# Kernel tuning notes

Measured on AMD Instinct MI355X. Metric: run time of the kernel, lower is better.

Reference implementation:

```python
import jax, jax.numpy as jnp
import numpy as np

N = 384          # nodes per graph
HID = 128        # hid_dim
H = 8            # shared_num_heads
C = HID // H     # shared_head_dim = 16
L = 4            # num_layers
VOCAB = 20
NORB = 4
NCAT = NORB * NORB + NORB   # 20 edge categories
OUT = 10
B = 4
E = N * N        # fully-connected closure incl. self loops
EPS = 1e-5


def layer_norm(x, g, b):
    m = jnp.mean(x, axis=-1, keepdims=True)
    v = jnp.mean((x - m) ** 2, axis=-1, keepdims=True)
    return (x - m) / jnp.sqrt(v + EPS) * g + b


def setup_inputs() -> dict:
    key = jax.random.key(0)
    ks = iter(jax.random.split(key, 32))

    def nrm(shape, s=0.05):
        return jax.random.normal(next(ks), shape, jnp.float32) * s

    # edge structure: fully connected, edge (i,j) in row-major order
    pos = np.arange(N) % NORB                    # node -> orbit
    src = np.repeat(np.arange(N), N)
    tgt = np.tile(np.arange(N), N)
    cat = np.where(src == tgt, NORB * NORB + pos[src], pos[src] * NORB + pos[tgt])

    x = jax.random.randint(next(ks), (B, N, 1), 0, VOCAB, jnp.int32)

    return dict(
        x=x,
        edge_src=jnp.asarray(src, jnp.int32),
        edge_tgt=jnp.asarray(tgt, jnp.int32),
        edge_cat=jnp.asarray(cat, jnp.int32),
        token_emb=nrm((VOCAB, HID), 1.0),
        edge_emb=nrm((NCAT, HID), 1.0),
        ln_in1_g=jnp.ones((HID,), jnp.float32), ln_in1_b=jnp.zeros((HID,), jnp.float32),
        W_in=nrm((HID, HID)), b_in=jnp.zeros((HID,), jnp.float32),
        ln_in2_g=jnp.ones((HID,), jnp.float32), ln_in2_b=jnp.zeros((HID,), jnp.float32),
        Wl=nrm((L, HID, H * C)), bl=jnp.zeros((L, H * C), jnp.float32),
        Wr=nrm((L, HID, H * C)), br=jnp.zeros((L, H * C), jnp.float32),
        We=nrm((L, HID, H * C)),                           # lin_edge has no bias in PyG GATv2Conv
        att=nrm((L, H, C)),
        bias_gat=jnp.zeros((L, H * C), jnp.float32),
        W_proj=nrm((L, HID, HID)), b_proj=jnp.zeros((L, HID), jnp.float32),
        ln_g=jnp.ones((L, HID), jnp.float32), ln_b=jnp.zeros((L, HID), jnp.float32),
        W_out=nrm((HID, OUT)), b_out=jnp.zeros((OUT,), jnp.float32),
    )


def reference(x, edge_src, edge_tgt, edge_cat,
              token_emb, edge_emb,
              ln_in1_g, ln_in1_b, W_in, b_in, ln_in2_g, ln_in2_b,
              Wl, bl, Wr, br, We, att, bias_gat,
              W_proj, b_proj, ln_g, ln_b, W_out, b_out):
    edge_feat = edge_emb[edge_cat]                       # [E, HID] gather by category
    h = token_emb[x[..., 0]]                             # [B, N, HID]
    # input MLP: LN -> ReLU -> Linear -> LN
    h = layer_norm(h, ln_in1_g, ln_in1_b)
    h = jax.nn.relu(h)
    h = h @ W_in + b_in
    h = layer_norm(h, ln_in2_g, ln_in2_b)

    for l in range(L):
        edge_e = (edge_feat @ We[l]).reshape(E, H, C)    # shared across batch

        def conv(hb):  # hb: [N, HID]  GATv2Conv, concat heads
            xl = (hb @ Wl[l] + bl[l]).reshape(N, H, C)   # source transform
            xr = (hb @ Wr[l] + br[l]).reshape(N, H, C)   # target transform
            e = jax.nn.leaky_relu(xl[edge_src] + xr[edge_tgt] + edge_e, 0.2)  # [E,H,C]
            logits = jnp.einsum('ehc,hc->eh', e, att[l])                      # [E,H]
            # segment softmax over edges sharing a target node
            m = jax.ops.segment_max(logits, edge_tgt, num_segments=N)
            ex = jnp.exp(logits - m[edge_tgt])
            den = jax.ops.segment_sum(ex, edge_tgt, num_segments=N)
            alpha = ex / den[edge_tgt]                                        # [E,H]
            out = jax.ops.segment_sum(xl[edge_src] * alpha[:, :, None], edge_tgt,
                                      num_segments=N)                         # [N,H,C]
            return out.reshape(N, H * C) + bias_gat[l]

        h_prev = h
        h = jax.vmap(conv)(h)                            # [B, N, HID]
        h = h @ W_proj[l] + b_proj[l]
        h = layer_norm(h, ln_g[l], ln_b[l])
        h = jax.nn.relu(h) + h_prev                      # residual

    h = h.sum(axis=1)                                    # sum over nodes -> [B, HID]
    return h @ W_out + b_out                             # [B, OUT]
```

## Files before the change

kernel.cpp:

```cpp
#include <hip/hip_runtime.h>


#define NN 384
#define NB 4
#define TJ 4

__device__ __forceinline__ void reduce64(float& a, float& b) {
#pragma unroll
  for (int m = 1; m <= 32; m <<= 1) {
    a += __shfl_xor(a, m, 64);
    b += __shfl_xor(b, m, 64);
  }
}

__global__ __launch_bounds__(256) void k_init(
    const int* __restrict__ x,
    const float* __restrict__ token_emb, const float* __restrict__ edge_emb,
    const float* __restrict__ ln1g, const float* __restrict__ ln1b,
    const float* __restrict__ W_in, const float* __restrict__ b_in,
    const float* __restrict__ ln2g, const float* __restrict__ ln2b,
    const float* __restrict__ Wl, const float* __restrict__ bl,
    const float* __restrict__ Wr, const float* __restrict__ br,
    const float* __restrict__ We, const float* __restrict__ att_w,
    float* __restrict__ ce, float* __restrict__ h,
    float* __restrict__ xl, float* __restrict__ xr, float* __restrict__ datt0)
{
  const int blk = blockIdx.x, t = threadIdx.x;
  if (blk < 40) {
    const int idx = blk * 256 + t;
    const int hc = idx & 127, rest = idx >> 7;
    const int cat = rest % 20, l = rest / 20;
    const float* er = edge_emb + cat * 128;
    const float* w  = We + (l * 128) * 128 + hc;
    float acc = 0.f;
#pragma unroll 8
    for (int k = 0; k < 128; ++k) acc = fmaf(er[k], w[k * 128], acc);
    ce[idx] = acc;
    return;
  }
  __shared__ float trow[4][128];
  __shared__ float hbuf[4][128];
  const int r0 = (blk - 40) * 4;
  const int r = t >> 6, c2 = (t & 63) * 2;
  const int row = r0 + r;
  const int tok = x[row];
  float2 v = *(const float2*)(token_emb + tok * 128 + c2);
  float s1 = v.x + v.y;
  float s2 = v.x * v.x + v.y * v.y;
  reduce64(s1, s2);
  float mean = s1 * 0.0078125f;
  float inv  = rsqrtf(s2 * 0.0078125f - mean * mean + 1e-5f);
  {
    float2 g  = *(const float2*)(ln1g + c2);
    float2 bb = *(const float2*)(ln1b + c2);
    trow[r][c2 + 0] = fmaxf((v.x - mean) * inv * g.x + bb.x, 0.f);
    trow[r][c2 + 1] = fmaxf((v.y - mean) * inv * g.y + bb.y, 0.f);
  }
  __syncthreads();
  const int o = t & 127, rh = (t >> 7) * 2;
  {
    float a0, a1;
    { float bo = b_in[o]; a0 = a1 = bo; }
    for (int k = 0; k < 128; ++k) {
      float w = W_in[k * 128 + o];
      a0 = fmaf(trow[rh + 0][k], w, a0);
      a1 = fmaf(trow[rh + 1][k], w, a1);
    }
    hbuf[rh + 0][o] = a0; hbuf[rh + 1][o] = a1;
  }
  __syncthreads();
  v = *(const float2*)(&hbuf[r][c2]);
  s1 = v.x + v.y;
  s2 = v.x * v.x + v.y * v.y;
  reduce64(s1, s2);
  mean = s1 * 0.0078125f;
  inv  = rsqrtf(s2 * 0.0078125f - mean * mean + 1e-5f);
  {
    float2 g  = *(const float2*)(ln2g + c2);
    float2 bb = *(const float2*)(ln2b + c2);
    float2 hv;
    hv.x = (v.x - mean) * inv * g.x + bb.x;
    hv.y = (v.y - mean) * inv * g.y + bb.y;
    trow[r][c2] = hv.x; trow[r][c2 + 1] = hv.y;
    *(float2*)(h + row * 128 + c2) = hv;
  }
  __syncthreads();
  const int m = t >> 7;
  const float* W = m ? Wr : Wl;
  const float bias = (m ? br : bl)[o];
  float a0 = bias, a1 = bias, a2 = bias, a3 = bias;
  for (int k = 0; k < 128; ++k) {
    float wv = W[k * 128 + o];
    a0 = fmaf(trow[0][k], wv, a0);
    a1 = fmaf(trow[1][k], wv, a1);
    a2 = fmaf(trow[2][k], wv, a2);
    a3 = fmaf(trow[3][k], wv, a3);
  }
  float* dst = m ? xr : xl;
  dst[(r0 + 0) * 128 + o] = a0;
  dst[(r0 + 1) * 128 + o] = a1;
  dst[(r0 + 2) * 128 + o] = a2;
  dst[(r0 + 3) * 128 + o] = a3;
  if (m == 0) {
    float av = att_w[o];
    float s0 = av * a0, sA = av * a1, sB = av * a2, sC = av * a3;
#pragma unroll
    for (int mm = 1; mm <= 8; mm <<= 1) {
      s0 += __shfl_xor(s0, mm, 64);
      sA += __shfl_xor(sA, mm, 64);
      sB += __shfl_xor(sB, mm, 64);
      sC += __shfl_xor(sC, mm, 64);
    }
    if ((t & 15) == 0) {
      const int hh2 = o >> 4;
      const int b2 = r0 / NN, ii = r0 - b2 * NN;
      const int base = (b2 * 8 + hh2) * NN + ii;
      datt0[base + 0] = s0; datt0[base + 1] = sA;
      datt0[base + 2] = sB; datt0[base + 3] = sC;
    }
  }
}

__global__ __launch_bounds__(256) void k_layer(
    const float* __restrict__ xl_in, const float* __restrict__ xr_in,
    const float* __restrict__ datt_in,
    float* __restrict__ xl_out, float* __restrict__ xr_out,
    float* __restrict__ datt_out,
    float* __restrict__ h, const float* __restrict__ ce,
    const float* __restrict__ att_w, const float* __restrict__ bias_gat,
    const float* __restrict__ W_proj, const float* __restrict__ b_proj,
    const float* __restrict__ ln_g, const float* __restrict__ ln_b,
    const float* __restrict__ Wl, const float* __restrict__ bl,
    const float* __restrict__ Wr, const float* __restrict__ br,
    int l, int next_l)
{
  __shared__ float xrce[TJ][5][136];
  __shared__ float djr02[TJ][5][8];
  __shared__ float mbuf[8][32][17];
  __shared__ float arow[TJ][132];
  __shared__ float pbuf[2 * TJ][132];
  __shared__ float nrow[TJ][132];

  const int t = threadIdx.x;
  const int jt = blockIdx.x, b = blockIdx.y;
  const int j0 = jt * TJ;

  for (int idx = t; idx < TJ * 5 * 128; idx += 256) {
    const int hc = idx & 127, rest = idx >> 7;
    const int sel = rest % 5, jj = rest / 5;
    const int j = j0 + jj, pj = j & 3;
    const int cat = (sel == 4) ? (16 + pj) : (sel * 4 + pj);
    xrce[jj][sel][hc] = xr_in[(b * NN + j) * 128 + hc]
                      + ce[(l * 20 + cat) * 128 + hc];
  }
  __syncthreads();
  if (t < TJ * 5 * 8) {
    const int jj = t / 40, r2 = t % 40, sel = r2 >> 3, h2 = r2 & 7;
    float d = 0.f;
#pragma unroll
    for (int c = 0; c < 16; ++c)
      d += xrce[jj][sel][h2 * 16 + c] * att_w[l * 128 + h2 * 16 + c];
    djr02[jj][sel][h2] = 0.2f * d;
  }
  __syncthreads();

  const int hh = t >> 5, isub = t & 31;
  float attv[16];
  {
    const float* ap = att_w + l * 128 + hh * 16;
#pragma unroll
    for (int c = 0; c < 16; ++c) attv[c] = ap[c];
  }
  float sden[TJ];
  float acc[TJ][16];
#pragma unroll
  for (int jj = 0; jj < TJ; ++jj) {
    sden[jj] = 0.f;
#pragma unroll
    for (int c = 0; c < 16; ++c) acc[jj][c] = 0.f;
  }
  const float* xlb = xl_in + (b * NN) * 128 + hh * 16;
  const float* dp  = datt_in + (b * 8 + hh) * NN;

#pragma unroll 2
  for (int it = 0; it < NN / 32; ++it) {
    const int i = isub + 32 * it;
    float xv[16];
    {
      const float4* xp = (const float4*)(xlb + i * 128);
#pragma unroll
      for (int q = 0; q < 4; ++q) {
        float4 a = xp[q];
        xv[q * 4 + 0] = a.x; xv[q * 4 + 1] = a.y;
        xv[q * 4 + 2] = a.z; xv[q * 4 + 3] = a.w;
      }
    }
    const float di02 = 0.2f * dp[i];
    const int pi = i & 3;
#pragma unroll
    for (int jj = 0; jj < TJ; ++jj) {
      const int sel = (i == j0 + jj) ? 4 : pi;
      const float4* bp = (const float4*)(&xrce[jj][sel][hh * 16]);
      float p = 0.f;
#pragma unroll
      for (int q = 0; q < 4; ++q) {
        float4 cv = bp[q];
        p = fmaf(fmaxf(xv[q * 4 + 0] + cv.x, 0.f), attv[q * 4 + 0], p);
        p = fmaf(fmaxf(xv[q * 4 + 1] + cv.y, 0.f), attv[q * 4 + 1], p);
        p = fmaf(fmaxf(xv[q * 4 + 2] + cv.z, 0.f), attv[q * 4 + 2], p);
        p = fmaf(fmaxf(xv[q * 4 + 3] + cv.w, 0.f), attv[q * 4 + 3], p);
      }
      const float e = __expf(fmaf(0.8f, p, di02 + djr02[jj][sel][hh]));
      sden[jj] += e;
#pragma unroll
      for (int c = 0; c < 16; ++c) acc[jj][c] = fmaf(e, xv[c], acc[jj][c]);
    }
  }

  {
    const int lc = isub & 15, up = isub >> 4;
#pragma unroll
    for (int jj = 0; jj < TJ; ++jj) {
      mbuf[hh][isub][0] = sden[jj];
#pragma unroll
      for (int c = 0; c < 16; ++c) mbuf[hh][isub][1 + c] = acc[jj][c];
      float nsum = 0.f, dsum = 0.f;
#pragma unroll 4
      for (int u2 = 0; u2 < 16; ++u2) {
        const int u = up * 16 + u2;
        dsum += mbuf[hh][u][0];
        nsum += mbuf[hh][u][1 + lc];
      }
      nsum += __shfl_xor(nsum, 16, 64); dsum += __shfl_xor(dsum, 16, 64);
      if (isub < 16)
        arow[jj][hh * 16 + isub] =
            nsum / dsum + bias_gat[l * 128 + hh * 16 + isub];
    }
  }
  __syncthreads();

  {
    const int o = t & 127, g4 = t >> 7;
    const float* Wp = W_proj + l * 16384;
    float p0 = 0.f, p1 = 0.f, p2 = 0.f, p3 = 0.f;
    const int k0 = g4 * 64;
    for (int kk = 0; kk < 64; ++kk) {
      const int k = k0 + kk;
      const float w = Wp[k * 128 + o];
      p0 = fmaf(arow[0][k], w, p0);
      p1 = fmaf(arow[1][k], w, p1);
      p2 = fmaf(arow[2][k], w, p2);
      p3 = fmaf(arow[3][k], w, p3);
    }
    pbuf[g4 * TJ + 0][o] = p0;
    pbuf[g4 * TJ + 1][o] = p1;
    pbuf[g4 * TJ + 2][o] = p2;
    pbuf[g4 * TJ + 3][o] = p3;
  }
  __syncthreads();
  for (int idx = t; idx < TJ * 128; idx += 256) {
    const int rr = idx >> 7, o = idx & 127;
    nrow[rr][o] = pbuf[rr][o] + pbuf[TJ + rr][o] + b_proj[l * 128 + o];
  }
  __syncthreads();

  {
    const int w = t >> 6;
    const int c2 = (t & 63) * 2;
    float v0 = nrow[w][c2], v1 = nrow[w][c2 + 1];
    float s1 = v0 + v1, s2 = v0 * v0 + v1 * v1;
#pragma unroll
    for (int m = 1; m <= 32; m <<= 1) {
      s1 += __shfl_xor(s1, m, 64);
      s2 += __shfl_xor(s2, m, 64);
    }
    const float mean = s1 * 0.0078125f;
    const float inv  = rsqrtf(s2 * 0.0078125f - mean * mean + 1e-5f);
    const int row = (b * NN + j0 + w) * 128;
    const float g0 = ln_g[l * 128 + c2], g1 = ln_g[l * 128 + c2 + 1];
    const float b0 = ln_b[l * 128 + c2], b1 = ln_b[l * 128 + c2 + 1];
    const float hp0 = h[row + c2], hp1 = h[row + c2 + 1];
    const float hn0 = fmaxf((v0 - mean) * inv * g0 + b0, 0.f) + hp0;
    const float hn1 = fmaxf((v1 - mean) * inv * g1 + b1, 0.f) + hp1;
    h[row + c2] = hn0; h[row + c2 + 1] = hn1;
    nrow[w][c2] = hn0; nrow[w][c2 + 1] = hn1;
  }
  __syncthreads();

  if (next_l >= 0) {
    const int o = t & 127, m = t >> 7;
    const float* W = (m ? Wr : Wl) + next_l * 16384;
    const float bias = (m ? br : bl)[next_l * 128 + o];
    float a0 = bias, a1 = bias, a2 = bias, a3 = bias;
    for (int k = 0; k < 128; ++k) {
      const float wv = W[k * 128 + o];
      a0 = fmaf(nrow[0][k], wv, a0);
      a1 = fmaf(nrow[1][k], wv, a1);
      a2 = fmaf(nrow[2][k], wv, a2);
      a3 = fmaf(nrow[3][k], wv, a3);
    }
    float* dst = m ? xr_out : xl_out;
    const int rb = (b * NN + j0) * 128 + o;
    dst[rb +   0] = a0; dst[rb + 128] = a1;
    dst[rb + 256] = a2; dst[rb + 384] = a3;
    if (m == 0) {
      const float av = att_w[next_l * 128 + o];
      float s0 = av * a0, s1 = av * a1, s2 = av * a2, s3 = av * a3;
#pragma unroll
      for (int mm = 1; mm <= 8; mm <<= 1) {
        s0 += __shfl_xor(s0, mm, 64);
        s1 += __shfl_xor(s1, mm, 64);
        s2 += __shfl_xor(s2, mm, 64);
        s3 += __shfl_xor(s3, mm, 64);
      }
      if ((t & 15) == 0) {
        const int base = (b * 8 + (o >> 4)) * NN + j0;
        datt_out[base + 0] = s0;
        datt_out[base + 1] = s1;
        datt_out[base + 2] = s2;
        datt_out[base + 3] = s3;
      }
    }
  }
}

__global__ __launch_bounds__(256) void k_final(
    const float* __restrict__ h, const float* __restrict__ W_out,
    const float* __restrict__ b_out, float* __restrict__ out)
{
  __shared__ float sbuf[2][128];
  const int bq = blockIdx.x, t = threadIdx.x;
  const int o = t & 127, half = t >> 7;
  float acc = 0.f;
  const float* hp = h + (bq * NN + half * 192) * 128 + o;
  for (int n = 0; n < 192; ++n) acc += hp[n * 128];
  sbuf[half][o] = acc;
  __syncthreads();
  if (t < 10) {
    float a = b_out[t];
#pragma unroll 8
    for (int k = 0; k < 128; ++k)
      a = fmaf(sbuf[0][k] + sbuf[1][k], W_out[k * 10 + t], a);
    out[bq * 10 + t] = a;
  }
}

extern "C" void kernel_launch(void* const* d_in, const int* in_sizes, int n_in,
                              void* d_out, int out_size, void* d_ws, size_t ws_size,
                              hipStream_t stream) {
  const int*   x         = (const int*)d_in[0];
  const float* token_emb = (const float*)d_in[4];
  const float* edge_emb  = (const float*)d_in[5];
  const float* ln1g      = (const float*)d_in[6];
  const float* ln1b      = (const float*)d_in[7];
  const float* W_in      = (const float*)d_in[8];
  const float* b_in      = (const float*)d_in[9];
  const float* ln2g      = (const float*)d_in[10];
  const float* ln2b      = (const float*)d_in[11];
  const float* Wl        = (const float*)d_in[12];
  const float* bl        = (const float*)d_in[13];
  const float* Wr        = (const float*)d_in[14];
  const float* br        = (const float*)d_in[15];
  const float* We        = (const float*)d_in[16];
  const float* att_w     = (const float*)d_in[17];
  const float* bias_gat  = (const float*)d_in[18];
  const float* W_proj    = (const float*)d_in[19];
  const float* b_proj    = (const float*)d_in[20];
  const float* ln_g      = (const float*)d_in[21];
  const float* ln_b      = (const float*)d_in[22];
  const float* W_out     = (const float*)d_in[23];
  const float* b_out     = (const float*)d_in[24];

  float* ws  = (float*)d_ws;
  float* ce  = ws;
  float* h   = ce  + 10240;
  float* xlA = h   + 196608;
  float* xrA = xlA + 196608;
  float* xlB = xrA + 196608;
  float* xrB = xlB + 196608;
  float* dA  = xrB + 196608;
  float* dB  = dA  + 12288;

  k_init<<<dim3(40 + 384), 256, 0, stream>>>(
      x, token_emb, edge_emb, ln1g, ln1b, W_in, b_in, ln2g, ln2b,
      Wl, bl, Wr, br, We, att_w, ce, h, xlA, xrA, dA);
  for (int l = 0; l < 4; ++l) {
    const bool even = (l & 1) == 0;
    float* xin  = even ? xlA : xlB;  float* rin  = even ? xrA : xrB;
    float* din  = even ? dA  : dB;
    float* xout = even ? xlB : xlA;  float* rout = even ? xrB : xrA;
    float* dout = even ? dB  : dA;
    k_layer<<<dim3(NN / TJ, NB), 256, 0, stream>>>(
        xin, rin, din, xout, rout, dout, h, ce, att_w, bias_gat,
        W_proj, b_proj, ln_g, ln_b, Wl, bl, Wr, br, l, (l < 3) ? l + 1 : -1);
  }
  k_final<<<dim3(NB), 256, 0, stream>>>(h, W_out, b_out, (float*)d_out);
}
```

Before: 236.9 us.

## Fuse init, layers and final into one persistent kernel with grid barriers

Merges the init kernel, the four per-layer kernels and the final reduction into a single persistent launch of 384 blocks. Stages are separated by a hand-written flag-based grid barrier built on agent-scope atomics. The goal is to remove the per-launch overhead and tail gaps of six kernel launches. The cost is barrier latency, and the design relies on all 384 blocks being co-resident (launch_bounds 256,2); without that the barrier could deadlock. It also needs flag reset at exit for the next call.

```diff
diff --git a/kernel.cpp b/kernel.cpp
--- a/kernel.cpp
+++ b/kernel.cpp
@@ -4,6 +4,36 @@
 #define NN 384
 #define NB 4
 #define TJ 4
+#define NJT 96
+#define NBLK 384
+
+__device__ unsigned g_flag[NBLK];
+__device__ unsigned g_rel;
+
+__device__ __forceinline__ void gridbar(int k, int blk, int t) {
+  __syncthreads();
+  __threadfence();
+  if (blk == 0) {
+    for (int s = 1 + t; s < NBLK; s += 256)
+      while (__hip_atomic_load(&g_flag[s], __ATOMIC_ACQUIRE,
+                               __HIP_MEMORY_SCOPE_AGENT) < (unsigned)k)
+        __builtin_amdgcn_s_sleep(2);
+    __syncthreads();
+    if (t == 0)
+      __hip_atomic_store(&g_rel, (unsigned)k, __ATOMIC_RELEASE,
+                         __HIP_MEMORY_SCOPE_AGENT);
+  } else {
+    if (t == 0) {
+      __hip_atomic_store(&g_flag[blk], (unsigned)k, __ATOMIC_RELEASE,
+                         __HIP_MEMORY_SCOPE_AGENT);
+      while (__hip_atomic_load(&g_rel, __ATOMIC_ACQUIRE,
+                               __HIP_MEMORY_SCOPE_AGENT) < (unsigned)k)
+        __builtin_amdgcn_s_sleep(2);
+    }
+  }
+  __syncthreads();
+  __threadfence();
+}
 
 __device__ __forceinline__ void reduce64(float& a, float& b) {
 #pragma unroll
@@ -13,7 +43,19 @@
   }
 }
 
-__global__ __launch_bounds__(256) void k_init(
+struct SmemLayer {
+  float xrce[TJ][5][136];
+  float djr02[TJ][5][8];
+  float mbuf[8][32][17];
+  float arow[TJ][132];
+  float pbuf[2 * TJ][132];
+  float nrow[TJ][132];
+};
+struct SmemInit  { float trow[4][128]; float hbuf[4][128]; };
+struct SmemFinal { float sbuf[2][128]; };
+union SmemU { SmemLayer L; SmemInit I; SmemFinal F; };
+
+__global__ __launch_bounds__(256, 2) void k_mega(
     const int* __restrict__ x,
     const float* __restrict__ token_emb, const float* __restrict__ edge_emb,
     const float* __restrict__ ln1g, const float* __restrict__ ln1b,
@@ -22,10 +64,24 @@
     const float* __restrict__ Wl, const float* __restrict__ bl,
     const float* __restrict__ Wr, const float* __restrict__ br,
     const float* __restrict__ We, const float* __restrict__ att_w,
-    float* __restrict__ ce, float* __restrict__ h,
-    float* __restrict__ xl, float* __restrict__ xr, float* __restrict__ datt0)
+    const float* __restrict__ bias_gat,
+    const float* __restrict__ W_proj, const float* __restrict__ b_proj,
+    const float* __restrict__ ln_g, const float* __restrict__ ln_b,
+    const float* __restrict__ W_out, const float* __restrict__ b_out,
+    float* __restrict__ ws, float* __restrict__ out)
 {
+  __shared__ SmemU smem;
+  float* ce  = ws;
+  float* h   = ce  + 10240;
+  float* xlA = h   + 196608;
+  float* xrA = xlA + 196608;
+  float* xlB = xrA + 196608;
+  float* xrB = xlB + 196608;
+  float* dA  = xrB + 196608;
+  float* dB  = dA  + 12288;
+
   const int blk = blockIdx.x, t = threadIdx.x;
+
   if (blk < 40) {
     const int idx = blk * 256 + t;
     const int hc = idx & 127, rest = idx >> 7;
@@ -36,312 +92,310 @@
 #pragma unroll 8
     for (int k = 0; k < 128; ++k) acc = fmaf(er[k], w[k * 128], acc);
     ce[idx] = acc;
-    return;
-  }
-  __shared__ float trow[4][128];
-  __shared__ float hbuf[4][128];
-  const int r0 = (blk - 40) * 4;
-  const int r = t >> 6, c2 = (t & 63) * 2;
-  const int row = r0 + r;
-  const int tok = x[row];
-  float2 v = *(const float2*)(token_emb + tok * 128 + c2);
-  float s1 = v.x + v.y;
-  float s2 = v.x * v.x + v.y * v.y;
-  reduce64(s1, s2);
-  float mean = s1 * 0.0078125f;
-  float inv  = rsqrtf(s2 * 0.0078125f - mean * mean + 1e-5f);
+  }
   {
-    float2 g  = *(const float2*)(ln1g + c2);
-    float2 bb = *(const float2*)(ln1b + c2);
-    trow[r][c2 + 0] = fmaxf((v.x - mean) * inv * g.x + bb.x, 0.f);
-    trow[r][c2 + 1] = fmaxf((v.y - mean) * inv * g.y + bb.y, 0.f);
-  }
-  __syncthreads();
-  const int o = t & 127, rh = (t >> 7) * 2;
-  {
-    float a0, a1;
-    { float bo = b_in[o]; a0 = a1 = bo; }
-    for (int k = 0; k < 128; ++k) {
-      float w = W_in[k * 128 + o];
-      a0 = fmaf(trow[rh + 0][k], w, a0);
-      a1 = fmaf(trow[rh + 1][k], w, a1);
-    }
-    hbuf[rh + 0][o] = a0; hbuf[rh + 1][o] = a1;
-  }
-  __syncthreads();
-  v = *(const float2*)(&hbuf[r][c2]);
-  s1 = v.x + v.y;
-  s2 = v.x * v.x + v.y * v.y;
-  reduce64(s1, s2);
-  mean = s1 * 0.0078125f;
-  inv  = rsqrtf(s2 * 0.0078125f - mean * mean + 1e-5f);
-  {
-    float2 g  = *(const float2*)(ln2g + c2);
-    float2 bb = *(const float2*)(ln2b + c2);
-    float2 hv;
-    hv.x = (v.x - mean) * inv * g.x + bb.x;
-    hv.y = (v.y - mean) * inv * g.y + bb.y;
-    trow[r][c2] = hv.x; trow[r][c2 + 1] = hv.y;
-    *(float2*)(h + row * 128 + c2) = hv;
-  }
-  __syncthreads();
-  const int m = t >> 7;
-  const float* W = m ? Wr : Wl;
-  const float bias = (m ? br : bl)[o];
-  float a0 = bias, a1 = bias, a2 = bias, a3 = bias;
-  for (int k = 0; k < 128; ++k) {
-    float wv = W[k * 128 + o];
-    a0 = fmaf(trow[0][k], wv, a0);
-    a1 = fmaf(trow[1][k], wv, a1);
-    a2 = fmaf(trow[2][k], wv, a2);
-    a3 = fmaf(trow[3][k], wv, a3);
-  }
-  float* dst = m ? xr : xl;
-  dst[(r0 + 0) * 128 + o] = a0;
-  dst[(r0 + 1) * 128 + o] = a1;
-  dst[(r0 + 2) * 128 + o] = a2;
-  dst[(r0 + 3) * 128 + o] = a3;
-  if (m == 0) {
-    float av = att_w[o];
-    float s0 = av * a0, sA = av * a1, sB = av * a2, sC = av * a3;
-#pragma unroll
-    for (int mm = 1; mm <= 8; mm <<= 1) {
-      s0 += __shfl_xor(s0, mm, 64);
-      sA += __shfl_xor(sA, mm, 64);
-      sB += __shfl_xor(sB, mm, 64);
-      sC += __shfl_xor(sC, mm, 64);
-    }
-    if ((t & 15) == 0) {
-      const int hh2 = o >> 4;
-      const int b2 = r0 / NN, ii = r0 - b2 * NN;
-      const int base = (b2 * 8 + hh2) * NN + ii;
-      datt0[base + 0] = s0; datt0[base + 1] = sA;
-      datt0[base + 2] = sB; datt0[base + 3] = sC;
-    }
-  }
-}
-
-__global__ __launch_bounds__(256) void k_layer(
-    const float* __restrict__ xl_in, const float* __restrict__ xr_in,
-    const float* __restrict__ datt_in,
-    float* __restrict__ xl_out, float* __restrict__ xr_out,
-    float* __restrict__ datt_out,
-    float* __restrict__ h, const float* __restrict__ ce,
-    const float* __restrict__ att_w, const float* __restrict__ bias_gat,
-    const float* __restrict__ W_proj, const float* __restrict__ b_proj,
-    const float* __restrict__ ln_g, const float* __restrict__ ln_b,
-    const float* __restrict__ Wl, const float* __restrict__ bl,
-    const float* __restrict__ Wr, const float* __restrict__ br,
-    int l, int next_l)
-{
-  __shared__ float xrce[TJ][5][136];
-  __shared__ float djr02[TJ][5][8];
-  __shared__ float mbuf[8][32][17];
-  __shared__ float arow[TJ][132];
-  __shared__ float pbuf[2 * TJ][132];
-  __shared__ float nrow[TJ][132];
-
-  const int t = threadIdx.x;
-  const int jt = blockIdx.x, b = blockIdx.y;
-  const int j0 = jt * TJ;
-
-  for (int idx = t; idx < TJ * 5 * 128; idx += 256) {
-    const int hc = idx & 127, rest = idx >> 7;
-    const int sel = rest % 5, jj = rest / 5;
-    const int j = j0 + jj, pj = j & 3;
-    const int cat = (sel == 4) ? (16 + pj) : (sel * 4 + pj);
-    xrce[jj][sel][hc] = xr_in[(b * NN + j) * 128 + hc]
-                      + ce[(l * 20 + cat) * 128 + hc];
-  }
-  __syncthreads();
-  if (t < TJ * 5 * 8) {
-    const int jj = t / 40, r2 = t % 40, sel = r2 >> 3, h2 = r2 & 7;
-    float d = 0.f;
-#pragma unroll
-    for (int c = 0; c < 16; ++c)
-      d += xrce[jj][sel][h2 * 16 + c] * att_w[l * 128 + h2 * 16 + c];
-    djr02[jj][sel][h2] = 0.2f * d;
-  }
-  __syncthreads();
-
-  const int hh = t >> 5, isub = t & 31;
-  float attv[16];
-  {
-    const float* ap = att_w + l * 128 + hh * 16;
-#pragma unroll
-    for (int c = 0; c < 16; ++c) attv[c] = ap[c];
-  }
-  float sden[TJ];
-  float acc[TJ][16];
-#pragma unroll
-  for (int jj = 0; jj < TJ; ++jj) {
-    sden[jj] = 0.f;
-#pragma unroll
-    for (int c = 0; c < 16; ++c) acc[jj][c] = 0.f;
-  }
-  const float* xlb = xl_in + (b * NN) * 128 + hh * 16;
-  const float* dp  = datt_in + (b * 8 + hh) * NN;
-
-#pragma unroll 2
-  for (int it = 0; it < NN / 32; ++it) {
-    const int i = isub + 32 * it;
-    float xv[16];
-    {
-      const float4* xp = (const float4*)(xlb + i * 128);
-#pragma unroll
-      for (int q = 0; q < 4; ++q) {
-        float4 a = xp[q];
-        xv[q * 4 + 0] = a.x; xv[q * 4 + 1] = a.y;
-        xv[q * 4 + 2] = a.z; xv[q * 4 + 3] = a.w;
-      }
-    }
-    const float di02 = 0.2f * dp[i];
-    const int pi = i & 3;
-#pragma unroll
-    for (int jj = 0; jj < TJ; ++jj) {
-      const int sel = (i == j0 + jj) ? 4 : pi;
-      const float4* bp = (const float4*)(&xrce[jj][sel][hh * 16]);
-      float p = 0.f;
-#pragma unroll
-      for (int q = 0; q < 4; ++q) {
-        float4 cv = bp[q];
-        p = fmaf(fmaxf(xv[q * 4 + 0] + cv.x, 0.f), attv[q * 4 + 0], p);
-        p = fmaf(fmaxf(xv[q * 4 + 1] + cv.y, 0.f), attv[q * 4 + 1], p);
-        p = fmaf(fmaxf(xv[q * 4 + 2] + cv.z, 0.f), attv[q * 4 + 2], p);
-        p = fmaf(fmaxf(xv[q * 4 + 3] + cv.w, 0.f), attv[q * 4 + 3], p);
-      }
-      const float e = __expf(fmaf(0.8f, p, di02 + djr02[jj][sel][hh]));
-      sden[jj] += e;
-#pragma unroll
-      for (int c = 0; c < 16; ++c) acc[jj][c] = fmaf(e, xv[c], acc[jj][c]);
-    }
-  }
-
-  {
-    const int lc = isub & 15, up = isub >> 4;
-#pragma unroll
-    for (int jj = 0; jj < TJ; ++jj) {
-      mbuf[hh][isub][0] = sden[jj];
-#pragma unroll
-      for (int c = 0; c < 16; ++c) mbuf[hh][isub][1 + c] = acc[jj][c];
-      float nsum = 0.f, dsum = 0.f;
-#pragma unroll 4
-      for (int u2 = 0; u2 < 16; ++u2) {
-        const int u = up * 16 + u2;
-        dsum += mbuf[hh][u][0];
-        nsum += mbuf[hh][u][1 + lc];
-      }
-      nsum += __shfl_xor(nsum, 16, 64); dsum += __shfl_xor(dsum, 16, 64);
-      if (isub < 16)
-        arow[jj][hh * 16 + isub] =
-            nsum / dsum + bias_gat[l * 128 + hh * 16 + isub];
-    }
-  }
-  __syncthreads();
-
-  {
-    const int o = t & 127, g4 = t >> 7;
-    const float* Wp = W_proj + l * 16384;
-    float p0 = 0.f, p1 = 0.f, p2 = 0.f, p3 = 0.f;
-    const int k0 = g4 * 64;
-    for (int kk = 0; kk < 64; ++kk) {
-      const int k = k0 + kk;
-      const float w = Wp[k * 128 + o];
-      p0 = fmaf(arow[0][k], w, p0);
-      p1 = fmaf(arow[1][k], w, p1);
-      p2 = fmaf(arow[2][k], w, p2);
-      p3 = fmaf(arow[3][k], w, p3);
-    }
-    pbuf[g4 * TJ + 0][o] = p0;
-    pbuf[g4 * TJ + 1][o] = p1;
-    pbuf[g4 * TJ + 2][o] = p2;
-    pbuf[g4 * TJ + 3][o] = p3;
-  }
-  __syncthreads();
-  for (int idx = t; idx < TJ * 128; idx += 256) {
-    const int rr = idx >> 7, o = idx & 127;
-    nrow[rr][o] = pbuf[rr][o] + pbuf[TJ + rr][o] + b_proj[l * 128 + o];
-  }
-  __syncthreads();
-
-  {
-    const int w = t >> 6;
-    const int c2 = (t & 63) * 2;
-    float v0 = nrow[w][c2], v1 = nrow[w][c2 + 1];
-    float s1 = v0 + v1, s2 = v0 * v0 + v1 * v1;
-#pragma unroll
-    for (int m = 1; m <= 32; m <<= 1) {
-      s1 += __shfl_xor(s1, m, 64);
-      s2 += __shfl_xor(s2, m, 64);
-    }
-    const float mean = s1 * 0.0078125f;
-    const float inv  = rsqrtf(s2 * 0.0078125f - mean * mean + 1e-5f);
-    const int row = (b * NN + j0 + w) * 128;
-    const float g0 = ln_g[l * 128 + c2], g1 = ln_g[l * 128 + c2 + 1];
-    const float b0 = ln_b[l * 128 + c2], b1 = ln_b[l * 128 + c2 + 1];
-    const float hp0 = h[row + c2], hp1 = h[row + c2 + 1];
-    const float hn0 = fmaxf((v0 - mean) * inv * g0 + b0, 0.f) + hp0;
-    const float hn1 = fmaxf((v1 - mean) * inv * g1 + b1, 0.f) + hp1;
-    h[row + c2] = hn0; h[row + c2 + 1] = hn1;
-    nrow[w][c2] = hn0; nrow[w][c2 + 1] = hn1;
-  }
-  __syncthreads();
-
-  if (next_l >= 0) {
-    const int o = t & 127, m = t >> 7;
-    const float* W = (m ? Wr : Wl) + next_l * 16384;
-    const float bias = (m ? br : bl)[next_l * 128 + o];
+    auto& I = smem.I;
+    const int r0 = blk * 4;
+    const int r = t >> 6, c2 = (t & 63) * 2;
+    const int row = r0 + r;
+    const int tok = x[row];
+    float2 v = *(const float2*)(token_emb + tok * 128 + c2);
+    float s1 = v.x + v.y;
+    float s2 = v.x * v.x + v.y * v.y;
+    reduce64(s1, s2);
+    float mean = s1 * 0.0078125f;
+    float inv  = rsqrtf(s2 * 0.0078125f - mean * mean + 1e-5f);
+    {
+      float2 g  = *(const float2*)(ln1g + c2);
+      float2 bb = *(const float2*)(ln1b + c2);
+      I.trow[r][c2 + 0] = fmaxf((v.x - mean) * inv * g.x + bb.x, 0.f);
+      I.trow[r][c2 + 1] = fmaxf((v.y - mean) * inv * g.y + bb.y, 0.f);
+    }
+    __syncthreads();
+    const int o = t & 127, rh = (t >> 7) * 2;
+    {
+      float a0, a1;
+      { float bo = b_in[o]; a0 = a1 = bo; }
+      for (int k = 0; k < 128; ++k) {
+        float w = W_in[k * 128 + o];
+        a0 = fmaf(I.trow[rh + 0][k], w, a0);
+        a1 = fmaf(I.trow[rh + 1][k], w, a1);
+      }
+      I.hbuf[rh + 0][o] = a0; I.hbuf[rh + 1][o] = a1;
+    }
+    __syncthreads();
+    v = *(const float2*)(&I.hbuf[r][c2]);
+    s1 = v.x + v.y;
+    s2 = v.x * v.x + v.y * v.y;
+    reduce64(s1, s2);
+    mean = s1 * 0.0078125f;
+    inv  = rsqrtf(s2 * 0.0078125f - mean * mean + 1e-5f);
+    {
+      float2 g  = *(const float2*)(ln2g + c2);
+      float2 bb = *(const float2*)(ln2b + c2);
+      float2 hv;
+      hv.x = (v.x - mean) * inv * g.x + bb.x;
+      hv.y = (v.y - mean) * inv * g.y + bb.y;
+      I.trow[r][c2] = hv.x; I.trow[r][c2 + 1] = hv.y;
+      *(float2*)(h + row * 128 + c2) = hv;
+    }
+    __syncthreads();
+    const int m = t >> 7;
+    const float* W = m ? Wr : Wl;
+    const float bias = (m ? br : bl)[o];
     float a0 = bias, a1 = bias, a2 = bias, a3 = bias;
     for (int k = 0; k < 128; ++k) {
-      const float wv = W[k * 128 + o];
-      a0 = fmaf(nrow[0][k], wv, a0);
-      a1 = fmaf(nrow[1][k], wv, a1);
-      a2 = fmaf(nrow[2][k], wv, a2);
-      a3 = fmaf(nrow[3][k], wv, a3);
-    }
-    float* dst = m ? xr_out : xl_out;
-    const int rb = (b * NN + j0) * 128 + o;
-    dst[rb +   0] = a0; dst[rb + 128] = a1;
-    dst[rb + 256] = a2; dst[rb + 384] = a3;
+      float wv = W[k * 128 + o];
+      a0 = fmaf(I.trow[0][k], wv, a0);
+      a1 = fmaf(I.trow[1][k], wv, a1);
+      a2 = fmaf(I.trow[2][k], wv, a2);
+      a3 = fmaf(I.trow[3][k], wv, a3);
+    }
+    float* dst = m ? xrA : xlA;
+    dst[(r0 + 0) * 128 + o] = a0;
+    dst[(r0 + 1) * 128 + o] = a1;
+    dst[(r0 + 2) * 128 + o] = a2;
+    dst[(r0 + 3) * 128 + o] = a3;
     if (m == 0) {
-      const float av = att_w[next_l * 128 + o];
-      float s0 = av * a0, s1 = av * a1, s2 = av * a2, s3 = av * a3;
+      float av = att_w[o];
+      float s0 = av * a0, sA = av * a1, sB = av * a2, sC = av * a3;
 #pragma unroll
       for (int mm = 1; mm <= 8; mm <<= 1) {
         s0 += __shfl_xor(s0, mm, 64);
-        s1 += __shfl_xor(s1, mm, 64);
-        s2 += __shfl_xor(s2, mm, 64);
-        s3 += __shfl_xor(s3, mm, 64);
+        sA += __shfl_xor(sA, mm, 64);
+        sB += __shfl_xor(sB, mm, 64);
+        sC += __shfl_xor(sC, mm, 64);
       }
       if ((t & 15) == 0) {
-        const int base = (b * 8 + (o >> 4)) * NN + j0;
-        datt_out[base + 0] = s0;
-        datt_out[base + 1] = s1;
-        datt_out[base + 2] = s2;
-        datt_out[base + 3] = s3;
-      }
-    }
-  }
-}
-
-__global__ __launch_bounds__(256) void k_final(
-    const float* __restrict__ h, const float* __restrict__ W_out,
-    const float* __restrict__ b_out, float* __restrict__ out)
-{
-  __shared__ float sbuf[2][128];
-  const int bq = blockIdx.x, t = threadIdx.x;
-  const int o = t & 127, half = t >> 7;
-  float acc = 0.f;
-  const float* hp = h + (bq * NN + half * 192) * 128 + o;
-  for (int n = 0; n < 192; ++n) acc += hp[n * 128];
-  sbuf[half][o] = acc;
+        const int hh2 = o >> 4;
+        const int b2 = r0 / NN, ii = r0 - b2 * NN;
+        const int base = (b2 * 8 + hh2) * NN + ii;
+        dA[base + 0] = s0; dA[base + 1] = sA;
+        dA[base + 2] = sB; dA[base + 3] = sC;
+      }
+    }
+  }
+  gridbar(1, blk, t);
+
+  auto& S = smem.L;
+  const int b = blk / NJT, jt = blk - b * NJT;
+  const int j0 = jt * TJ;
+  const int hh = t >> 5, isub = t & 31;
+
+#pragma unroll 1
+  for (int l = 0; l < 4; ++l) {
+    const int next_l = (l < 3) ? l + 1 : -1;
+    float* xl_in   = (l & 1) ? xlB : xlA;
+    float* xr_in   = (l & 1) ? xrB : xrA;
+    float* datt_in = (l & 1) ? dB  : dA;
+    float* xl_out  = (l & 1) ? xlA : xlB;
+    float* xr_out  = (l & 1) ? xrA : xrB;
+    float* datt_out= (l & 1) ? dA  : dB;
+
+    for (int idx = t; idx < TJ * 5 * 128; idx += 256) {
+      const int hc = idx & 127, rest = idx >> 7;
+      const int sel = rest % 5, jj = rest / 5;
+      const int j = j0 + jj, pj = j & 3;
+      const int cat = (sel == 4) ? (16 + pj) : (sel * 4 + pj);
+      S.xrce[jj][sel][hc] = xr_in[(b * NN + j) * 128 + hc]
+                          + ce[(l * 20 + cat) * 128 + hc];
+    }
+    __syncthreads();
+    if (t < TJ * 5 * 8) {
+      const int jj = t / 40, r2 = t % 40, sel = r2 >> 3, h2 = r2 & 7;
+      float d = 0.f;
+#pragma unroll
+      for (int c = 0; c < 16; ++c)
+        d += S.xrce[jj][sel][h2 * 16 + c] * att_w[l * 128 + h2 * 16 + c];
+      S.djr02[jj][sel][h2] = 0.2f * d;
+    }
+    __syncthreads();
+
+    float attv[16];
+    {
+      const float* ap = att_w + l * 128 + hh * 16;
+#pragma unroll
+      for (int c = 0; c < 16; ++c) attv[c] = ap[c];
+    }
+    float sden[TJ];
+    float acc[TJ][16];
+#pragma unroll
+    for (int jj = 0; jj < TJ; ++jj) {
+      sden[jj] = 0.f;
+#pragma unroll
+      for (int c = 0; c < 16; ++c) acc[jj][c] = 0.f;
+    }
+    const float* xlb = xl_in + (b * NN) * 128 + hh * 16;
+    const float* dp  = datt_in + (b * 8 + hh) * NN;
+
+#pragma unroll 2
+    for (int it = 0; it < NN / 32; ++it) {
+      const int i = isub + 32 * it;
+      float xv[16];
+      {
+        const float4* xp = (const float4*)(xlb + i * 128);
+#pragma unroll
+        for (int q = 0; q < 4; ++q) {
+          float4 a = xp[q];
+          xv[q * 4 + 0] = a.x; xv[q * 4 + 1] = a.y;
+          xv[q * 4 + 2] = a.z; xv[q * 4 + 3] = a.w;
+        }
+      }
+      const float di02 = 0.2f * dp[i];
+      const int pi = i & 3;
+#pragma unroll
+      for (int jj = 0; jj < TJ; ++jj) {
+        const int sel = (i == j0 + jj) ? 4 : pi;
+        const float4* bp = (const float4*)(&S.xrce[jj][sel][hh * 16]);
+        float p = 0.f;
+#pragma unroll
+        for (int q = 0; q < 4; ++q) {
+          float4 cv = bp[q];
+          p = fmaf(fmaxf(xv[q * 4 + 0] + cv.x, 0.f), attv[q * 4 + 0], p);
+          p = fmaf(fmaxf(xv[q * 4 + 1] + cv.y, 0.f), attv[q * 4 + 1], p);
+          p = fmaf(fmaxf(xv[q * 4 + 2] + cv.z, 0.f), attv[q * 4 + 2], p);
+          p = fmaf(fmaxf(xv[q * 4 + 3] + cv.w, 0.f), attv[q * 4 + 3], p);
+        }
+        const float e = __expf(fmaf(0.8f, p, di02 + S.djr02[jj][sel][hh]));
+        sden[jj] += e;
+#pragma unroll
+        for (int c = 0; c < 16; ++c) acc[jj][c] = fmaf(e, xv[c], acc[jj][c]);
+      }
+    }
+
+    {
+      const int lc = isub & 15, up = isub >> 4;
+#pragma unroll
+      for (int jj = 0; jj < TJ; ++jj) {
+        S.mbuf[hh][isub][0] = sden[jj];
+#pragma unroll
+        for (int c = 0; c < 16; ++c) S.mbuf[hh][isub][1 + c] = acc[jj][c];
+        float nsum = 0.f, dsum = 0.f;
+#pragma unroll 4
+        for (int u2 = 0; u2 < 16; ++u2) {
+          const int u = up * 16 + u2;
+          dsum += S.mbuf[hh][u][0];
+          nsum += S.mbuf[hh][u][1 + lc];
+        }
+        nsum += __shfl_xor(nsum, 16, 64); dsum += __shfl_xor(dsum, 16, 64);
+        if (isub < 16)
+          S.arow[jj][hh * 16 + isub] =
+              nsum / dsum + bias_gat[l * 128 + hh * 16 + isub];
+      }
+    }
+    __syncthreads();
+
+    {
+      const int o = t & 127, g4 = t >> 7;
+      const float* Wp = W_proj + l * 16384;
+      float p0 = 0.f, p1 = 0.f, p2 = 0.f, p3 = 0.f;
+      const int k0 = g4 * 64;
+      for (int kk = 0; kk < 64; ++kk) {
+        const int k = k0 + kk;
+        const float w = Wp[k * 128 + o];
+        p0 = fmaf(S.arow[0][k], w, p0);
+        p1 = fmaf(S.arow[1][k], w, p1);
+        p2 = fmaf(S.arow[2][k], w, p2);
+        p3 = fmaf(S.arow[3][k], w, p3);
+      }
+      S.pbuf[g4 * TJ + 0][o] = p0;
+      S.pbuf[g4 * TJ + 1][o] = p1;
+      S.pbuf[g4 * TJ + 2][o] = p2;
+      S.pbuf[g4 * TJ + 3][o] = p3;
+    }
+    __syncthreads();
+    for (int idx = t; idx < TJ * 128; idx += 256) {
+      const int rr = idx >> 7, o = idx & 127;
+      S.nrow[rr][o] = S.pbuf[rr][o] + S.pbuf[TJ + rr][o] + b_proj[l * 128 + o];
+    }
+    __syncthreads();
+
+    {
+      const int w = t >> 6;
+      const int c2 = (t & 63) * 2;
+      float v0 = S.nrow[w][c2], v1 = S.nrow[w][c2 + 1];
+      float s1 = v0 + v1, s2 = v0 * v0 + v1 * v1;
+#pragma unroll
+      for (int m = 1; m <= 32; m <<= 1) {
+        s1 += __shfl_xor(s1, m, 64);
+        s2 += __shfl_xor(s2, m, 64);
+      }
+      const float mean = s1 * 0.0078125f;
+      const float inv  = rsqrtf(s2 * 0.0078125f - mean * mean + 1e-5f);
+      const int row = (b * NN + j0 + w) * 128;
+      const float g0 = ln_g[l * 128 + c2], g1 = ln_g[l * 128 + c2 + 1];
+      const float b0 = ln_b[l * 128 + c2], b1 = ln_b[l * 128 + c2 + 1];
+      const float hp0 = h[row + c2], hp1 = h[row + c2 + 1];
+      const float hn0 = fmaxf((v0 - mean) * inv * g0 + b0, 0.f) + hp0;
+      const float hn1 = fmaxf((v1 - mean) * inv * g1 + b1, 0.f) + hp1;
+      h[row + c2] = hn0; h[row + c2 + 1] = hn1;
+      S.nrow[w][c2] = hn0; S.nrow[w][c2 + 1] = hn1;
+    }
+    __syncthreads();
+
+    if (next_l >= 0) {
+      const int o = t & 127, m = t >> 7;
+      const float* W = (m ? Wr : Wl) + next_l * 16384;
+      const float bias = (m ? br : bl)[next_l * 128 + o];
+      float a0 = bias, a1 = bias, a2 = bias, a3 = bias;
+      for (int k = 0; k < 128; ++k) {
+        const float wv = W[k * 128 + o];
+        a0 = fmaf(S.nrow[0][k], wv, a0);
+        a1 = fmaf(S.nrow[1][k], wv, a1);
+        a2 = fmaf(S.nrow[2][k], wv, a2);
+        a3 = fmaf(S.nrow[3][k], wv, a3);
+      }
+      float* dst = m ? xr_out : xl_out;
+      const int rb = (b * NN + j0) * 128 + o;
+      dst[rb +   0] = a0; dst[rb + 128] = a1;
+      dst[rb + 256] = a2; dst[rb + 384] = a3;
+      if (m == 0) {
+        const float av = att_w[next_l * 128 + o];
+        float s0 = av * a0, s1 = av * a1, s2 = av * a2, s3 = av * a3;
+#pragma unroll
+        for (int mm = 1; mm <= 8; mm <<= 1) {
+          s0 += __shfl_xor(s0, mm, 64);
+          s1 += __shfl_xor(s1, mm, 64);
+          s2 += __shfl_xor(s2, mm, 64);
+          s3 += __shfl_xor(s3, mm, 64);
+        }
+        if ((t & 15) == 0) {
+          const int base = (b * 8 + (o >> 4)) * NN + j0;
+          datt_out[base + 0] = s0;
+          datt_out[base + 1] = s1;
+          datt_out[base + 2] = s2;
+          datt_out[base + 3] = s3;
+        }
+      }
+    }
+    gridbar(2 + l, blk, t);
+  }
+
+  if (blk < NB) {
+    auto& F = smem.F;
+    const int o = t & 127, half = t >> 7;
+    float accf = 0.f;
+    const float* hp = h + (blk * NN + half * 192) * 128 + o;
+    for (int n = 0; n < 192; ++n) accf += hp[n * 128];
+    F.sbuf[half][o] = accf;
+    __syncthreads();
+    if (t < 10) {
+      float a = b_out[t];
+#pragma unroll 8
+      for (int k = 0; k < 128; ++k)
+        a = fmaf(F.sbuf[0][k] + F.sbuf[1][k], W_out[k * 10 + t], a);
+      out[blk * 10 + t] = a;
+    }
+  }
+
   __syncthreads();
-  if (t < 10) {
-    float a = b_out[t];
-#pragma unroll 8
-    for (int k = 0; k < 128; ++k)
-      a = fmaf(sbuf[0][k] + sbuf[1][k], W_out[k * 10 + t], a);
-    out[bq * 10 + t] = a;
+  if (t == 0) {
+    if (blk == 0)
+      __hip_atomic_store(&g_rel, 0u, __ATOMIC_RELAXED,
+                         __HIP_MEMORY_SCOPE_AGENT);
+    else
+      __hip_atomic_store(&g_flag[blk], 0u, __ATOMIC_RELAXED,
+                         __HIP_MEMORY_SCOPE_AGENT);
   }
 }
 
@@ -371,28 +425,8 @@
   const float* W_out     = (const float*)d_in[23];
   const float* b_out     = (const float*)d_in[24];
 
-  float* ws  = (float*)d_ws;
-  float* ce  = ws;
-  float* h   = ce  + 10240;
-  float* xlA = h   + 196608;
-  float* xrA = xlA + 196608;
-  float* xlB = xrA + 196608;
-  float* xrB = xlB + 196608;
-  float* dA  = xrB + 196608;
-  float* dB  = dA  + 12288;
-
-  k_init<<<dim3(40 + 384), 256, 0, stream>>>(
+  k_mega<<<dim3(NBLK), 256, 0, stream>>>(
       x, token_emb, edge_emb, ln1g, ln1b, W_in, b_in, ln2g, ln2b,
-      Wl, bl, Wr, br, We, att_w, ce, h, xlA, xrA, dA);
-  for (int l = 0; l < 4; ++l) {
-    const bool even = (l & 1) == 0;
-    float* xin  = even ? xlA : xlB;  float* rin  = even ? xrA : xrB;
-    float* din  = even ? dA  : dB;
-    float* xout = even ? xlB : xlA;  float* rout = even ? xrB : xrA;
-    float* dout = even ? dB  : dA;
-    k_layer<<<dim3(NN / TJ, NB), 256, 0, stream>>>(
-        xin, rin, din, xout, rout, dout, h, ce, att_w, bias_gat,
-        W_proj, b_proj, ln_g, ln_b, Wl, bl, Wr, br, l, (l < 3) ? l + 1 : -1);
-  }
-  k_final<<<dim3(NB), 256, 0, stream>>>(h, W_out, b_out, (float*)d_out);
+      Wl, bl, Wr, br, We, att_w, bias_gat, W_proj, b_proj, ln_g, ln_b,
+      W_out, b_out, (float*)d_ws, (float*)d_out);
 }
```

Measured after the change: 816.5 us. 3.45x slower.
